# Kernel tuning notes

Measured on AMD Instinct MI355X. Metric: run time of the kernel, lower is better.

## Reference

```python
import jax, jax.numpy as jnp
import numpy as np
from jax import lax

B, S, T = 32, 128, 64          # batch, src_len, trg_len
E, H = 64, 512                 # embed_dim, hidden_size
SRC_V, TRG_V = 32000, 32000


def gru_cell(x, h, W_ih, W_hh, b_ih, b_hh):
    """PyTorch-convention GRU cell. x:[B,I], h:[B,H] -> h':[B,H]"""
    gi = x @ W_ih.T + b_ih            # [B,3H]
    gh = h @ W_hh.T + b_hh            # [B,3H]
    i_r, i_z, i_n = jnp.split(gi, 3, axis=-1)
    h_r, h_z, h_n = jnp.split(gh, 3, axis=-1)
    r = jax.nn.sigmoid(i_r + h_r)
    z = jax.nn.sigmoid(i_z + h_z)
    n = jnp.tanh(i_n + r * h_n)
    return (1.0 - z) * n + z * h


def setup_inputs() -> dict:
    key = jax.random.key(0)
    ks = jax.random.split(key, 22)
    g = lambda i, shape: jax.random.normal(ks[i], shape, jnp.float32) * 0.05
    return {
        "src": jax.random.randint(ks[0], (B, S), 0, SRC_V),
        "trg": jax.random.randint(ks[1], (B, T), 0, TRG_V),
        "src_embed": g(2, (SRC_V, E)),
        "trg_embed": g(3, (TRG_V, E)),
        # encoder GRU (1 layer, input E)
        "enc_W_ih": g(4, (3 * H, E)), "enc_W_hh": g(5, (3 * H, H)),
        "enc_b_ih": g(6, (3 * H,)), "enc_b_hh": g(7, (3 * H,)),
        # decoder GRU layer 0 (input E+H due to attention concat)
        "dec0_W_ih": g(8, (3 * H, E + H)), "dec0_W_hh": g(9, (3 * H, H)),
        "dec0_b_ih": g(10, (3 * H,)), "dec0_b_hh": g(11, (3 * H,)),
        # decoder GRU layer 1 (input H)
        "dec1_W_ih": g(12, (3 * H, H)), "dec1_W_hh": g(13, (3 * H, H)),
        "dec1_b_ih": g(14, (3 * H,)), "dec1_b_hh": g(15, (3 * H,)),
        # additive attention: energy = tanh(W[h;enc]) , score = v^T energy
        "attn_W": g(16, (H, 2 * H)), "attn_b": g(17, (H,)),
        "v_W": g(18, (1, H)), "v_b": jnp.zeros((1,), jnp.float32),
        # output projection H -> TRG_V
        "fc_W": g(19, (TRG_V, H)), "fc_b": jnp.zeros((TRG_V,), jnp.float32),
    }


def reference(src, trg, src_embed, trg_embed,
              enc_W_ih, enc_W_hh, enc_b_ih, enc_b_hh,
              dec0_W_ih, dec0_W_hh, dec0_b_ih, dec0_b_hh,
              dec1_W_ih, dec1_W_hh, dec1_b_ih, dec1_b_hh,
              attn_W, attn_b, v_W, v_b, fc_W, fc_b):
    batch = src.shape[0]
    src_e = src_embed[src]                              # [B,S,E]

    # ---- encoder: 1-layer GRU over src ----
    def enc_step(h, x):
        h2 = gru_cell(x, h, enc_W_ih, enc_W_hh, enc_b_ih, enc_b_hh)
        return h2, h2
    h0 = jnp.zeros((batch, H), src_e.dtype)
    h_last, enc_outs = lax.scan(enc_step, h0, jnp.swapaxes(src_e, 0, 1))
    enc_outs = jnp.swapaxes(enc_outs, 0, 1)             # [B,S,H]

    # _adapt_hidden: replicate last encoder layer to 2 decoder layers
    carry0 = (h_last, h_last)

    # ---- decoder: teacher forcing (ratio=1.0), steps t=1..T-1 ----
    def dec_step(carry, tok):
        h0_, h1_ = carry
        # attention context from top decoder layer hidden
        q = jnp.concatenate(
            [jnp.broadcast_to(h1_[:, None, :], enc_outs.shape), enc_outs], axis=-1)  # [B,S,2H]
        energy = jnp.tanh(q @ attn_W.T + attn_b)        # [B,S,H]
        scores = energy @ v_W[0] + v_b[0]               # [B,S]
        w = jax.nn.softmax(scores, axis=-1)
        context = jnp.einsum('bs,bsh->bh', w, enc_outs) # [B,H]
        emb = jnp.concatenate([trg_embed[tok], context], axis=-1)  # [B,E+H]
        h0n = gru_cell(emb, h0_, dec0_W_ih, dec0_W_hh, dec0_b_ih, dec0_b_hh)
        h1n = gru_cell(h0n, h1_, dec1_W_ih, dec1_W_hh, dec1_b_ih, dec1_b_hh)
        logits = h1n @ fc_W.T + fc_b                    # [B,V]
        return (h0n, h1n), logits

    tokens = jnp.swapaxes(trg[:, :-1], 0, 1)            # inputs for t=1..T-1
    _, logits = lax.scan(dec_step, carry0, tokens)      # [T-1,B,V]
    outputs = jnp.concatenate(
        [jnp.zeros((batch, 1, TRG_V), logits.dtype), jnp.swapaxes(logits, 0, 1)], axis=1)
    return outputs                                       # [B,T,V]
```

## Files before the change

kernel.cpp:

```cpp
#include <hip/hip_runtime.h>
#include <hip/hip_bf16.h>

#define BB 32
#define SS 128
#define TT 64
#define EE 64
#define HH 512
#define H3 1536
#define VV 32000
#define EHD 576
#define TD 63
#define MFC 2048

typedef unsigned short u16;
typedef unsigned int   u32;

typedef __attribute__((ext_vector_type(8))) short bf16x8;
typedef __attribute__((ext_vector_type(4))) float f32x4;

__device__ __forceinline__ float bf2f(u16 u){ return __uint_as_float(((u32)u)<<16); }
__device__ __forceinline__ u16 f2bf(float f){
  u32 u = __float_as_uint(f);
  u += 0x7FFFu + ((u>>16)&1u);
  return (u16)(u>>16);
}
__device__ __forceinline__ float sigm(float x){ return 1.f/(1.f+__expf(-x)); }
__device__ __forceinline__ float tanh_f(float x){ return 1.f - 2.f/(1.f+__expf(2.f*x)); }

__device__ __forceinline__ void bf8f(uint4 q, float* f){
  f[0]=__uint_as_float(q.x<<16); f[1]=__uint_as_float(q.x&0xFFFF0000u);
  f[2]=__uint_as_float(q.y<<16); f[3]=__uint_as_float(q.y&0xFFFF0000u);
  f[4]=__uint_as_float(q.z<<16); f[5]=__uint_as_float(q.z&0xFFFF0000u);
  f[6]=__uint_as_float(q.w<<16); f[7]=__uint_as_float(q.w&0xFFFF0000u);
}

template<bool BF>
__device__ __forceinline__ void wload8(const void* base, size_t eoff, float* f){
  if constexpr (BF){
    uint4 q = *(const uint4*)((const u16*)base + eoff);
    bf8f(q, f);
  } else {
    const float4* p = (const float4*)((const float*)base + eoff);
    float4 a = p[0], b = p[1];
    f[0]=a.x; f[1]=a.y; f[2]=a.z; f[3]=a.w;
    f[4]=b.x; f[5]=b.y; f[6]=b.z; f[7]=b.w;
  }
}
template<bool BF>
__device__ __forceinline__ float wld(const void* base, size_t eoff){
  if constexpr (BF) return bf2f(((const u16*)base)[eoff]);
  else              return ((const float*)base)[eoff];
}
template<bool BF>
__device__ __forceinline__ void stage32(const void* gbase, size_t eoff, u16* lds){
  if constexpr (BF){
    const uint4* g = (const uint4*)((const u16*)gbase + eoff);
    uint4* l = (uint4*)lds;
    l[0]=g[0]; l[1]=g[1]; l[2]=g[2]; l[3]=g[3];
  } else {
    const float4* g = (const float4*)((const float*)gbase + eoff);
    #pragma unroll
    for(int i=0;i<8;i++){
      float4 v = g[i];
      u16* d = lds + i*4;
      d[0]=f2bf(v.x); d[1]=f2bf(v.y); d[2]=f2bf(v.z); d[3]=f2bf(v.w);
    }
  }
}

__device__ __forceinline__ void bbar(unsigned int* ctr, int tid, unsigned int target){
  __syncthreads();
  if(tid==0){
    __hip_atomic_fetch_add(ctr, 1u, __ATOMIC_RELEASE, __HIP_MEMORY_SCOPE_AGENT);
    while(__hip_atomic_load(ctr, __ATOMIC_RELAXED, __HIP_MEMORY_SCOPE_AGENT) < target){
      __builtin_amdgcn_s_sleep(1);
    }
    __builtin_amdgcn_fence(__ATOMIC_ACQUIRE, "agent");
  }
  __syncthreads();
}

__global__ __launch_bounds__(64) void k_detect(const void* w, int* flag){
  int tid = threadIdx.x;
  const u16* p = (const u16*)w;
  float m = 0.f;
  #pragma unroll
  for(int i=0;i<16;i++){
    float v = fabsf(bf2f(p[tid*16+i]));
    m = fmaxf(m, v);
  }
  #pragma unroll
  for(int off=32;off;off>>=1) m = fmaxf(m, __shfl_down(m, off));
  if(tid==0) *flag = (m < 16.f) ? 1 : 0;
}

template<bool BF>
__device__ void emb_gi_body(const int* toks, int tstride, const void* emb_tab,
                            const void* W_ih, int wstride, const void* b_ih,
                            float* gi)
{
  int blk = blockIdx.x;
  int jc = blk % 6; int b = (blk/6) % BB; int t = blk/(6*BB);
  int tid = threadIdx.x;
  int tok = toks[b*tstride + t];
  __shared__ float emb[EE];
  if(tid < EE) emb[tid] = wld<BF>(emb_tab, (size_t)tok*EE + tid);
  __syncthreads();
  int j = jc*256 + tid;
  float acc = wld<BF>(b_ih, j);
  size_t roff = (size_t)j*wstride;
  #pragma unroll
  for(int i=0;i<8;i++){
    float f[8]; wload8<BF>(W_ih, roff + i*8, f);
    #pragma unroll
    for(int l=0;l<8;l++) acc += emb[i*8+l]*f[l];
  }
  gi[((size_t)t*BB + b)*H3 + j] = acc;
}
__global__ __launch_bounds__(256) void k_emb_gi(
    const int* flag, const int* toks, int tstride, const void* emb_tab,
    const void* W_ih, int wstride, const void* b_ih, float* gi)
{
  if(*flag) emb_gi_body<true>(toks,tstride,emb_tab,W_ih,wstride,b_ih,gi);
  else      emb_gi_body<false>(toks,tstride,emb_tab,W_ih,wstride,b_ih,gi);
}

struct SMem {
  union {
    struct {
      float a[HH];
      float b[HH];
      float red[6][256];
      float eS[16];
    };
    float es16[16][520];
  };
};

struct EncDecParams {
  const int* flag;
  const void *eWhh, *ebhh;
  const float* enc_gi;
  float* enc_outs;
  const void *aW, *ab, *vW, *vb;
  const void *d0Wih, *d0Whh, *d0bhh;
  const float* trg_gi;
  const void *d1Wih, *d1bih, *d1Whh, *d1bhh;
  float* hE;
  float* h0b;
  float* h1b;
  float* P;
  float* Abuf;
  float* Cpart;
  float* Ssum;
  u16* h1_all;
  unsigned int* bctr;
};

template<bool BF>
__device__ void enc_step_dev(SMem& sm, int b, int q, int tid,
                             const float* hin, float* hout,
                             const void* W_hh, const void* b_hh,
                             const float* gi_t, float* enc_outs, int t,
                             float* h0init, float* h1init)
{
  float* hs = sm.b;
  const float* hrow = hin + b*HH;
  hs[tid] = hrow[tid]; hs[tid+256] = hrow[tid+256];
  __syncthreads();
  int jj = tid >> 2, t4 = tid & 3;
  int j = q*64 + jj;
  int k0 = t4*128;
  float ar=0.f, az=0.f, an=0.f;
  size_t orr = (size_t)j*HH + k0;
  size_t oz = (size_t)(512+j)*HH + k0;
  size_t on = (size_t)(1024+j)*HH + k0;
  #pragma unroll 4
  for(int i=0;i<16;i++){
    float f[8];
    wload8<BF>(W_hh, orr + i*8, f);
    #pragma unroll
    for(int l=0;l<8;l++) ar += hs[k0+i*8+l]*f[l];
    wload8<BF>(W_hh, oz + i*8, f);
    #pragma unroll
    for(int l=0;l<8;l++) az += hs[k0+i*8+l]*f[l];
    wload8<BF>(W_hh, on + i*8, f);
    #pragma unroll
    for(int l=0;l<8;l++) an += hs[k0+i*8+l]*f[l];
  }
  sm.red[0][tid]=ar; sm.red[1][tid]=az; sm.red[2][tid]=an;
  __syncthreads();
  if(t4==0){
    float gr = sm.red[0][tid]+sm.red[0][tid+1]+sm.red[0][tid+2]+sm.red[0][tid+3] + wld<BF>(b_hh, j);
    float gz = sm.red[1][tid]+sm.red[1][tid+1]+sm.red[1][tid+2]+sm.red[1][tid+3] + wld<BF>(b_hh, 512+j);
    float gn = sm.red[2][tid]+sm.red[2][tid+1]+sm.red[2][tid+2]+sm.red[2][tid+3] + wld<BF>(b_hh, 1024+j);
    const float* gib = gi_t + b*H3;
    float r = sigm(gib[j] + gr);
    float z = sigm(gib[512+j] + gz);
    float n = tanh_f(gib[1024+j] + r*gn);
    float hn = (1.f - z)*n + z*hs[j];
    hout[b*HH + j] = hn;
    enc_outs[((size_t)b*SS + t)*HH + j] = hn;
    if(h0init){ h0init[b*HH+j] = hn; h1init[b*HH+j] = hn; }
  }
}

template<bool BF>
__device__ void attn_proj_blk(SMem& sm, int b, int q, int tid,
                              const float* enc_outs, const void* attn_W,
                              const void* attn_b, float* P)
{
  #pragma unroll 4
  for(int i=0;i<16;i++){
    const float* er = enc_outs + ((size_t)b*SS + q*16 + i)*HH;
    sm.es16[i][tid]     = er[tid];
    sm.es16[i][tid+256] = er[tid+256];
  }
  __syncthreads();
  #pragma unroll
  for(int rr=0; rr<2; rr++){
    int j = rr*256 + tid;
    float bj = wld<BF>(attn_b, j);
    float acc[16];
    #pragma unroll
    for(int i=0;i<16;i++) acc[i] = bj;
    size_t roff = (size_t)j*1024 + 512;
    for(int kk=0;kk<64;kk++){
      float f[8]; wload8<BF>(attn_W, roff + kk*8, f);
      #pragma unroll
      for(int i=0;i<16;i++){
        const float4* e4 = (const float4*)(&sm.es16[i][kk*8]);
        float4 ea = e4[0], eb = e4[1];
        acc[i] += ea.x*f[0]+ea.y*f[1]+ea.z*f[2]+ea.w*f[3]
                + eb.x*f[4]+eb.y*f[5]+eb.z*f[6]+eb.w*f[7];
      }
    }
    #pragma unroll
    for(int i=0;i<16;i++)
      P[((size_t)b*SS + q*16 + i)*HH + j] = acc[i];
  }
  __syncthreads();
}

template<bool BF>
__device__ void dec_A_dev(SMem& sm, int b, int q, int tid,
                          const float* h1, const void* attn_W, float* Abuf)
{
  float* hsr = sm.b;
  hsr[tid]=h1[b*HH+tid]; hsr[tid+256]=h1[b*HH+tid+256];
  __syncthreads();
  int jj = tid>>2, t4 = tid&3, j = q*64+jj, k0 = t4*128;
  size_t roff = (size_t)j*1024 + k0;
  float acc = 0.f;
  #pragma unroll 4
  for(int i=0;i<16;i++){
    float f[8]; wload8<BF>(attn_W, roff + i*8, f);
    #pragma unroll
    for(int l=0;l<8;l++) acc += hsr[k0+i*8+l]*f[l];
  }
  sm.red[0][tid]=acc;
  __syncthreads();
  if(t4==0){
    Abuf[b*HH + j] = sm.red[0][tid]+sm.red[0][tid+1]+sm.red[0][tid+2]+sm.red[0][tid+3];
  }
}

template<bool BF>
__device__ void dec_scores_dev(SMem& sm, int b, int sb, int tid,
                               const float* Abuf, const float* P,
                               const float* enc_outs, const void* vW,
                               const void* vb, float* Cpart, float* Ssum)
{
  float* As = sm.a;
  float* vs = sm.b;
  As[tid]=Abuf[b*HH+tid]; As[tid+256]=Abuf[b*HH+tid+256];
  vs[tid]=wld<BF>(vW, tid); vs[tid+256]=wld<BF>(vW, tid+256);
  __syncthreads();
  int wave = tid>>6, lane = tid&63;
  float vbf = wld<BF>(vb, 0);
  #pragma unroll
  for(int i=0;i<4;i++){
    int s = sb*16 + wave*4 + i;
    const float* Prow = P + ((size_t)b*SS+s)*HH;
    float part = 0.f;
    #pragma unroll
    for(int kk=0;kk<8;kk++){
      int k = lane + kk*64;
      part += vs[k]*tanh_f(As[k]+Prow[k]);
    }
    #pragma unroll
    for(int off=32;off;off>>=1) part += __shfl_down(part, off);
    if(lane==0) sm.eS[wave*4+i] = __expf(part + vbf);
  }
  __syncthreads();
  for(int j=tid;j<HH;j+=256){
    float c = 0.f;
    #pragma unroll 4
    for(int i=0;i<16;i++) c += sm.eS[i]*enc_outs[((size_t)b*SS + sb*16+i)*HH + j];
    Cpart[((size_t)b*8+sb)*HH + j] = c;
  }
  if(tid==0){ float ss=0.f; for(int i=0;i<16;i++) ss+=sm.eS[i]; Ssum[b*8+sb]=ss; }
}

template<bool BF>
__device__ void dec_h0_dev(SMem& sm, int b, int q, int tid,
                           const float* h0in, float* h0out,
                           const float* Cpart, const float* Ssum,
                           const void* W_ih, const void* W_hh,
                           const void* b_hh, const float* gi_t)
{
  float* ctx = sm.a;
  float* hs  = sm.b;
  const float* hr = h0in + b*HH;
  hs[tid]=hr[tid]; hs[tid+256]=hr[tid+256];
  float ssum = 0.f;
  #pragma unroll
  for(int sb=0;sb<8;sb++) ssum += Ssum[b*8+sb];
  float invS = 1.f/ssum;
  for(int j=tid;j<HH;j+=256){
    float c = 0.f;
    #pragma unroll
    for(int sb=0;sb<8;sb++) c += Cpart[((size_t)b*8+sb)*HH + j];
    ctx[j] = c*invS;
  }
  __syncthreads();
  int jj = tid>>2, t4 = tid&3, j = q*64+jj, k0 = t4*128;
  float pr=0.f,pz=0.f,pn=0.f,qr=0.f,qz=0.f,qn=0.f;
  size_t oir = (size_t)j*EHD + 64 + k0;
  size_t oiz = (size_t)(512+j)*EHD + 64 + k0;
  size_t oin = (size_t)(1024+j)*EHD + 64 + k0;
  size_t ohr = (size_t)j*HH + k0;
  size_t ohz = (size_t)(512+j)*HH + k0;
  size_t ohn = (size_t)(1024+j)*HH + k0;
  #pragma unroll 2
  for(int i=0;i<16;i++){
    float f[8];
    wload8<BF>(W_ih, oir + i*8, f);
    #pragma unroll
    for(int l=0;l<8;l++) pr += ctx[k0+i*8+l]*f[l];
    wload8<BF>(W_ih, oiz + i*8, f);
    #pragma unroll
    for(int l=0;l<8;l++) pz += ctx[k0+i*8+l]*f[l];
    wload8<BF>(W_ih, oin + i*8, f);
    #pragma unroll
    for(int l=0;l<8;l++) pn += ctx[k0+i*8+l]*f[l];
    wload8<BF>(W_hh, ohr + i*8, f);
    #pragma unroll
    for(int l=0;l<8;l++) qr += hs[k0+i*8+l]*f[l];
    wload8<BF>(W_hh, ohz + i*8, f);
    #pragma unroll
    for(int l=0;l<8;l++) qz += hs[k0+i*8+l]*f[l];
    wload8<BF>(W_hh, ohn + i*8, f);
    #pragma unroll
    for(int l=0;l<8;l++) qn += hs[k0+i*8+l]*f[l];
  }
  sm.red[0][tid]=pr; sm.red[1][tid]=pz; sm.red[2][tid]=pn;
  sm.red[3][tid]=qr; sm.red[4][tid]=qz; sm.red[5][tid]=qn;
  __syncthreads();
  if(t4==0){
    float gir = gi_t[b*H3 + j]        + sm.red[0][tid]+sm.red[0][tid+1]+sm.red[0][tid+2]+sm.red[0][tid+3];
    float giz = gi_t[b*H3 + 512 + j]  + sm.red[1][tid]+sm.red[1][tid+1]+sm.red[1][tid+2]+sm.red[1][tid+3];
    float gin = gi_t[b*H3 + 1024 + j] + sm.red[2][tid]+sm.red[2][tid+1]+sm.red[2][tid+2]+sm.red[2][tid+3];
    float ghr = sm.red[3][tid]+sm.red[3][tid+1]+sm.red[3][tid+2]+sm.red[3][tid+3] + wld<BF>(b_hh, j);
    float ghz = sm.red[4][tid]+sm.red[4][tid+1]+sm.red[4][tid+2]+sm.red[4][tid+3] + wld<BF>(b_hh, 512+j);
    float ghn = sm.red[5][tid]+sm.red[5][tid+1]+sm.red[5][tid+2]+sm.red[5][tid+3] + wld<BF>(b_hh, 1024+j);
    float r = sigm(gir+ghr), z = sigm(giz+ghz), n = tanh_f(gin + r*ghn);
    h0out[b*HH + j] = (1.f - z)*n + z*hs[j];
  }
}

template<bool BF>
__device__ void dec_h1_dev(SMem& sm, int b, int q, int tid,
                           const float* xin, const float* h1in, float* h1out,
                           const void* W_ih, const void* b_ih,
                           const void* W_hh, const void* b_hh,
                           u16* h1_all_t)
{
  float* xs = sm.a;
  float* hs = sm.b;
  const float* xr = xin + b*HH;
  const float* hr = h1in + b*HH;
  xs[tid]=xr[tid]; xs[tid+256]=xr[tid+256];
  hs[tid]=hr[tid]; hs[tid+256]=hr[tid+256];
  __syncthreads();
  int jj = tid>>2, t4 = tid&3, j = q*64+jj, k0 = t4*128;
  float pr=0.f,pz=0.f,pn=0.f,qr=0.f,qz=0.f,qn=0.f;
  size_t oir = (size_t)j*HH + k0;
  size_t oiz = (size_t)(512+j)*HH + k0;
  size_t oin = (size_t)(1024+j)*HH + k0;
  #pragma unroll 2
  for(int i=0;i<16;i++){
    float f[8];
    wload8<BF>(W_ih, oir + i*8, f);
    #pragma unroll
    for(int l=0;l<8;l++) pr += xs[k0+i*8+l]*f[l];
    wload8<BF>(W_ih, oiz + i*8, f);
    #pragma unroll
    for(int l=0;l<8;l++) pz += xs[k0+i*8+l]*f[l];
    wload8<BF>(W_ih, oin + i*8, f);
    #pragma unroll
    for(int l=0;l<8;l++) pn += xs[k0+i*8+l]*f[l];
    wload8<BF>(W_hh, oir + i*8, f);
    #pragma unroll
    for(int l=0;l<8;l++) qr += hs[k0+i*8+l]*f[l];
    wload8<BF>(W_hh, oiz + i*8, f);
    #pragma unroll
    for(int l=0;l<8;l++) qz += hs[k0+i*8+l]*f[l];
    wload8<BF>(W_hh, oin + i*8, f);
    #pragma unroll
    for(int l=0;l<8;l++) qn += hs[k0+i*8+l]*f[l];
  }
  sm.red[0][tid]=pr; sm.red[1][tid]=pz; sm.red[2][tid]=pn;
  sm.red[3][tid]=qr; sm.red[4][tid]=qz; sm.red[5][tid]=qn;
  __syncthreads();
  if(t4==0){
    float gir = wld<BF>(b_ih, j)      + sm.red[0][tid]+sm.red[0][tid+1]+sm.red[0][tid+2]+sm.red[0][tid+3];
    float giz = wld<BF>(b_ih, 512+j)  + sm.red[1][tid]+sm.red[1][tid+1]+sm.red[1][tid+2]+sm.red[1][tid+3];
    float gin = wld<BF>(b_ih, 1024+j) + sm.red[2][tid]+sm.red[2][tid+1]+sm.red[2][tid+2]+sm.red[2][tid+3];
    float ghr = sm.red[3][tid]+sm.red[3][tid+1]+sm.red[3][tid+2]+sm.red[3][tid+3] + wld<BF>(b_hh, j);
    float ghz = sm.red[4][tid]+sm.red[4][tid+1]+sm.red[4][tid+2]+sm.red[4][tid+3] + wld<BF>(b_hh, 512+j);
    float ghn = sm.red[5][tid]+sm.red[5][tid+1]+sm.red[5][tid+2]+sm.red[5][tid+3] + wld<BF>(b_hh, 1024+j);
    float r = sigm(gir+ghr), z = sigm(giz+ghz), n = tanh_f(gin + r*ghn);
    float hn = (1.f - z)*n + z*hs[j];
    h1out[b*HH + j] = hn;
    h1_all_t[b*HH + j] = f2bf(hn);
  }
}

template<bool BF>
__device__ void encdec_body(const EncDecParams& p, SMem& sm)
{
  int blk = blockIdx.x, tid = threadIdx.x;
  int b = blk & 31, q = blk >> 5;
  unsigned int* ctr = p.bctr + b*64;
  unsigned int bt = 0;

  for(int t=0;t<SS;t++){
    enc_step_dev<BF>(sm, b, q, tid,
        p.hE + (t&1)*BB*HH, p.hE + ((t+1)&1)*BB*HH,
        p.eWhh, p.ebhh, p.enc_gi + (size_t)t*BB*H3, p.enc_outs, t,
        (t==SS-1)? p.h0b : (float*)nullptr,
        (t==SS-1)? p.h1b : (float*)nullptr);
    bt += 8; bbar(ctr, tid, bt);
  }

  attn_proj_blk<BF>(sm, b, q, tid, p.enc_outs, p.aW, p.ab, p.P);
  bt += 8; bbar(ctr, tid, bt);

  for(int t=0;t<TD;t++){
    int pi = t&1, po = (t+1)&1;
    dec_A_dev<BF>(sm, b, q, tid, p.h1b + pi*BB*HH, p.aW, p.Abuf);
    bt += 8; bbar(ctr, tid, bt);
    dec_scores_dev<BF>(sm, b, q, tid, p.Abuf, p.P, p.enc_outs, p.vW, p.vb,
                       p.Cpart, p.Ssum);
    bt += 8; bbar(ctr, tid, bt);
    dec_h0_dev<BF>(sm, b, q, tid, p.h0b + pi*BB*HH, p.h0b + po*BB*HH,
                   p.Cpart, p.Ssum, p.d0Wih, p.d0Whh, p.d0bhh,
                   p.trg_gi + (size_t)t*BB*H3);
    bt += 8; bbar(ctr, tid, bt);
    dec_h1_dev<BF>(sm, b, q, tid, p.h0b + po*BB*HH, p.h1b + pi*BB*HH,
                   p.h1b + po*BB*HH, p.d1Wih, p.d1bih, p.d1Whh, p.d1bhh,
                   p.h1_all + (size_t)t*BB*HH);
    bt += 8; bbar(ctr, tid, bt);
  }
}

__global__ __launch_bounds__(256) void k_encdec(EncDecParams p)
{
  __shared__ SMem sm;
  if(*p.flag) encdec_body<true>(p, sm);
  else        encdec_body<false>(p, sm);
}

__global__ __launch_bounds__(256) void k_zero_t0(const int* flag, void* out){
  int idx = blockIdx.x*256 + threadIdx.x;
  int b = idx / VV, v = idx - b*VV;
  size_t o = (size_t)b*TT*VV + v;
  if(*flag) ((u16*)out)[o] = 0;
  else      ((float*)out)[o] = 0.f;
}

template<bool BF>
__device__ void fc_body(const u16* A, const void* W, const void* bias, void* out)
{
  __shared__ u16 As[128*72];
  __shared__ u16 Bs[128*72];
  int bm = blockIdx.x, bn = blockIdx.y;
  int tid = threadIdx.x;
  int wave = tid>>6, lane = tid&63;
  int wr = wave>>1, wc = wave&1;
  f32x4 acc[4][4];
  f32x4 zero = {0.f,0.f,0.f,0.f};
  #pragma unroll
  for(int i=0;i<4;i++)
    #pragma unroll
    for(int j=0;j<4;j++) acc[i][j]=zero;

  int row = tid>>1, half = tid&1;
  const size_t gA = (size_t)(bm*128 + row)*512 + half*32;
  const size_t gB = (size_t)(bn*128 + row)*512 + half*32;
  u16* lA = As + row*72 + half*32;
  u16* lB = Bs + row*72 + half*32;

  for(int kk=0;kk<8;kk++){
    int k0 = kk*64;
    if(kk) __syncthreads();
    stage32<true>(A, gA + k0, lA);
    stage32<BF>(W, gB + k0, lB);
    __syncthreads();
    #pragma unroll
    for(int ks=0;ks<2;ks++){
      int kof = ks*32 + (lane>>4)*8;
      bf16x8 af[4], bfv[4];
      #pragma unroll
      for(int i=0;i<4;i++){
        af[i]  = *(const bf16x8*)(As + (wr*64 + i*16 + (lane&15))*72 + kof);
        bfv[i] = *(const bf16x8*)(Bs + (wc*64 + i*16 + (lane&15))*72 + kof);
      }
      #pragma unroll
      for(int i=0;i<4;i++)
        #pragma unroll
        for(int j=0;j<4;j++)
          acc[i][j] = __builtin_amdgcn_mfma_f32_16x16x32_bf16(af[i], bfv[j], acc[i][j], 0, 0, 0);
    }
  }
  int quad = lane>>4, col = lane&15;
  #pragma unroll
  for(int j=0;j<4;j++){
    int n = bn*128 + wc*64 + j*16 + col;
    float bsv = wld<BF>(bias, n);
    #pragma unroll
    for(int i=0;i<4;i++){
      int mbase = bm*128 + wr*64 + i*16 + quad*4;
      #pragma unroll
      for(int r=0;r<4;r++){
        int m = mbase + r;
        if(m < TD*BB){
          int t = m >> 5, b = m & 31;
          size_t o = ((size_t)(b*TT + t + 1))*VV + n;
          float v = acc[i][j][r] + bsv;
          if constexpr (BF) ((u16*)out)[o] = f2bf(v);
          else              ((float*)out)[o] = v;
        }
      }
    }
  }
}
__global__ __launch_bounds__(256) void k_fc(
  const int* flag, const u16* A, const void* W, const void* bias, void* out)
{
  if(*flag) fc_body<true>(A, W, bias, out);
  else      fc_body<false>(A, W, bias, out);
}

extern "C" void kernel_launch(void* const* d_in, const int* in_sizes, int n_in,
                              void* d_out, int out_size, void* d_ws, size_t ws_size,
                              hipStream_t stream)
{
  const int* src = (const int*)d_in[0];
  const int* trg = (const int*)d_in[1];
  const void* src_emb = d_in[2];
  const void* trg_emb = d_in[3];
  const void* eWih = d_in[4];
  const void* eWhh = d_in[5];
  const void* ebih = d_in[6];
  const void* ebhh = d_in[7];
  const void* d0Wih = d_in[8];
  const void* d0Whh = d_in[9];
  const void* d0bih = d_in[10];
  const void* d0bhh = d_in[11];
  const void* d1Wih = d_in[12];
  const void* d1Whh = d_in[13];
  const void* d1bih = d_in[14];
  const void* d1bhh = d_in[15];
  const void* aW  = d_in[16];
  const void* ab  = d_in[17];
  const void* vW  = d_in[18];
  const void* vb  = d_in[19];
  const void* fcW = d_in[20];
  const void* fcb = d_in[21];

  char* w = (char*)d_ws;
  int*   flag    = (int*)w;   w += 16;
  float* enc_gi  = (float*)w; w += (size_t)SS*BB*H3*4;
  float* trg_gi  = (float*)w; w += (size_t)TD*BB*H3*4;
  float* enc_outs= (float*)w; w += (size_t)BB*SS*HH*4;
  float* P       = (float*)w; w += (size_t)BB*SS*HH*4;
  float* hE      = (float*)w; w += (size_t)2*BB*HH*4;
  float* h0b     = (float*)w; w += (size_t)2*BB*HH*4;
  float* h1b     = (float*)w; w += (size_t)2*BB*HH*4;
  float* Abuf    = (float*)w; w += (size_t)BB*HH*4;
  float* Cpart   = (float*)w; w += (size_t)BB*8*HH*4;
  float* Ssum    = (float*)w; w += (size_t)BB*8*4;
  u16*   h1_all  = (u16*)w;   w += (size_t)MFC*HH*2;
  unsigned int* bctr = (unsigned int*)w; w += (size_t)BB*64*4;

  (void)hipMemsetAsync(hE, 0, BB*HH*4, stream);
  (void)hipMemsetAsync(h1_all + (size_t)TD*BB*HH, 0, 32*HH*2, stream);
  (void)hipMemsetAsync(bctr, 0, (size_t)BB*64*4, stream);

  k_detect<<<1,64,0,stream>>>(fcW, flag);

  k_emb_gi<<<SS*BB*6, 256, 0, stream>>>(flag, src, SS, src_emb, eWih, EE, ebih, enc_gi);
  k_emb_gi<<<TD*BB*6, 256, 0, stream>>>(flag, trg, TT, trg_emb, d0Wih, EHD, d0bih, trg_gi);

  EncDecParams prm;
  prm.flag = flag;
  prm.eWhh = eWhh; prm.ebhh = ebhh;
  prm.enc_gi = enc_gi;
  prm.enc_outs = enc_outs;
  prm.aW = aW; prm.ab = ab; prm.vW = vW; prm.vb = vb;
  prm.d0Wih = d0Wih; prm.d0Whh = d0Whh; prm.d0bhh = d0bhh;
  prm.trg_gi = trg_gi;
  prm.d1Wih = d1Wih; prm.d1bih = d1bih; prm.d1Whh = d1Whh; prm.d1bhh = d1bhh;
  prm.hE = hE; prm.h0b = h0b; prm.h1b = h1b;
  prm.P = P; prm.Abuf = Abuf; prm.Cpart = Cpart; prm.Ssum = Ssum;
  prm.h1_all = h1_all;
  prm.bctr = bctr;

  void* kargs[] = { (void*)&prm };
  (void)hipLaunchCooperativeKernel(reinterpret_cast<void*>(&k_encdec),
                                   dim3(256), dim3(256), kargs, 0, stream);

  k_zero_t0<<<(BB*VV)/256, 256, 0, stream>>>(flag, d_out);
  dim3 g(16, 250);
  k_fc<<<g, 256, 0, stream>>>(flag, h1_all, fcW, fcb, d_out);
}
```

Baseline: 8.419 ms.

## Use atomic agent-scope loads with workgroup fence, pad LDS, regroup batch blocks

Cross-block data (hidden states, enc_outs, Cpart, Ssum, Abuf) is now read with relaxed agent-scope 64-bit atomic loads. This lets the barrier's acquire fence be weakened from agent to workgroup scope, avoiding a full L2/cache invalidate on every step barrier. Shared hidden-state arrays are padded by 8 floats per 128 to remove LDS bank conflicts when four lanes read different k-segments. Block-to-batch mapping changes so the 8 blocks of one batch are contiguous, likely so they land on nearby CUs/XCDs. The catch is that correctness now depends on every cross-block read going through the atomic loads, and any plain load left behind could observe stale data.

```diff
diff --git a/kernel.cpp b/kernel.cpp
--- a/kernel.cpp
+++ b/kernel.cpp
@@ -68,6 +68,19 @@
   }
 }
 
+__device__ __forceinline__ float2 cld2(const float* p){
+  unsigned long long u = __hip_atomic_load((const unsigned long long*)p,
+                                           __ATOMIC_RELAXED, __HIP_MEMORY_SCOPE_AGENT);
+  float2 r;
+  r.x = __uint_as_float((u32)u);
+  r.y = __uint_as_float((u32)(u>>32));
+  return r;
+}
+__device__ __forceinline__ float cld1(const float* p){
+  u32 u = __hip_atomic_load((const u32*)p, __ATOMIC_RELAXED, __HIP_MEMORY_SCOPE_AGENT);
+  return __uint_as_float(u);
+}
+
 __device__ __forceinline__ void bbar(unsigned int* ctr, int tid, unsigned int target){
   __syncthreads();
   if(tid==0){
@@ -75,7 +88,7 @@
     while(__hip_atomic_load(ctr, __ATOMIC_RELAXED, __HIP_MEMORY_SCOPE_AGENT) < target){
       __builtin_amdgcn_s_sleep(1);
     }
-    __builtin_amdgcn_fence(__ATOMIC_ACQUIRE, "agent");
+    __builtin_amdgcn_fence(__ATOMIC_ACQUIRE, "workgroup");
   }
   __syncthreads();
 }
@@ -128,8 +141,8 @@
 struct SMem {
   union {
     struct {
-      float a[HH];
-      float b[HH];
+      float a[544];
+      float b[544];
       float red[6][256];
       float eS[16];
     };
@@ -165,12 +178,16 @@
                              float* h0init, float* h1init)
 {
   float* hs = sm.b;
-  const float* hrow = hin + b*HH;
-  hs[tid] = hrow[tid]; hs[tid+256] = hrow[tid+256];
+  {
+    float2 h2 = cld2(hin + b*HH + 2*tid);
+    int sk = ((2*tid)>>7)<<3;
+    hs[2*tid+sk] = h2.x; hs[2*tid+1+sk] = h2.y;
+  }
   __syncthreads();
   int jj = tid >> 2, t4 = tid & 3;
   int j = q*64 + jj;
   int k0 = t4*128;
+  const float* hsb = hs + t4*136;
   float ar=0.f, az=0.f, an=0.f;
   size_t orr = (size_t)j*HH + k0;
   size_t oz = (size_t)(512+j)*HH + k0;
@@ -180,13 +197,13 @@
     float f[8];
     wload8<BF>(W_hh, orr + i*8, f);
     #pragma unroll
-    for(int l=0;l<8;l++) ar += hs[k0+i*8+l]*f[l];
+    for(int l=0;l<8;l++) ar += hsb[i*8+l]*f[l];
     wload8<BF>(W_hh, oz + i*8, f);
     #pragma unroll
-    for(int l=0;l<8;l++) az += hs[k0+i*8+l]*f[l];
+    for(int l=0;l<8;l++) az += hsb[i*8+l]*f[l];
     wload8<BF>(W_hh, on + i*8, f);
     #pragma unroll
-    for(int l=0;l<8;l++) an += hs[k0+i*8+l]*f[l];
+    for(int l=0;l<8;l++) an += hsb[i*8+l]*f[l];
   }
   sm.red[0][tid]=ar; sm.red[1][tid]=az; sm.red[2][tid]=an;
   __syncthreads();
@@ -198,7 +215,8 @@
     float r = sigm(gib[j] + gr);
     float z = sigm(gib[512+j] + gz);
     float n = tanh_f(gib[1024+j] + r*gn);
-    float hn = (1.f - z)*n + z*hs[j];
+    int jsk = j + ((j>>7)<<3);
+    float hn = (1.f - z)*n + z*hs[jsk];
     hout[b*HH + j] = hn;
     enc_outs[((size_t)b*SS + t)*HH + j] = hn;
     if(h0init){ h0init[b*HH+j] = hn; h1init[b*HH+j] = hn; }
@@ -213,8 +231,9 @@
   #pragma unroll 4
   for(int i=0;i<16;i++){
     const float* er = enc_outs + ((size_t)b*SS + q*16 + i)*HH;
-    sm.es16[i][tid]     = er[tid];
-    sm.es16[i][tid+256] = er[tid+256];
+    float2 v = cld2(er + 2*tid);
+    sm.es16[i][2*tid]   = v.x;
+    sm.es16[i][2*tid+1] = v.y;
   }
   __syncthreads();
   #pragma unroll
@@ -247,16 +266,21 @@
                           const float* h1, const void* attn_W, float* Abuf)
 {
   float* hsr = sm.b;
-  hsr[tid]=h1[b*HH+tid]; hsr[tid+256]=h1[b*HH+tid+256];
+  {
+    float2 h2 = cld2(h1 + b*HH + 2*tid);
+    int sk = ((2*tid)>>7)<<3;
+    hsr[2*tid+sk] = h2.x; hsr[2*tid+1+sk] = h2.y;
+  }
   __syncthreads();
   int jj = tid>>2, t4 = tid&3, j = q*64+jj, k0 = t4*128;
+  const float* hsrb = hsr + t4*136;
   size_t roff = (size_t)j*1024 + k0;
   float acc = 0.f;
   #pragma unroll 4
   for(int i=0;i<16;i++){
     float f[8]; wload8<BF>(attn_W, roff + i*8, f);
     #pragma unroll
-    for(int l=0;l<8;l++) acc += hsr[k0+i*8+l]*f[l];
+    for(int l=0;l<8;l++) acc += hsrb[i*8+l]*f[l];
   }
   sm.red[0][tid]=acc;
   __syncthreads();
@@ -273,7 +297,10 @@
 {
   float* As = sm.a;
   float* vs = sm.b;
-  As[tid]=Abuf[b*HH+tid]; As[tid+256]=Abuf[b*HH+tid+256];
+  {
+    float2 a2 = cld2(Abuf + b*HH + 2*tid);
+    As[2*tid]=a2.x; As[2*tid+1]=a2.y;
+  }
   vs[tid]=wld<BF>(vW, tid); vs[tid+256]=wld<BF>(vW, tid+256);
   __syncthreads();
   int wave = tid>>6, lane = tid&63;
@@ -293,11 +320,16 @@
     if(lane==0) sm.eS[wave*4+i] = __expf(part + vbf);
   }
   __syncthreads();
-  for(int j=tid;j<HH;j+=256){
-    float c = 0.f;
-    #pragma unroll 4
-    for(int i=0;i<16;i++) c += sm.eS[i]*enc_outs[((size_t)b*SS + sb*16+i)*HH + j];
-    Cpart[((size_t)b*8+sb)*HH + j] = c;
+  {
+    float c0=0.f, c1=0.f;
+    const float* eb0 = enc_outs + ((size_t)b*SS + sb*16)*HH + 2*tid;
+    #pragma unroll
+    for(int i=0;i<16;i++){
+      float2 v = cld2(eb0 + (size_t)i*HH);
+      c0 += sm.eS[i]*v.x; c1 += sm.eS[i]*v.y;
+    }
+    float* cp = Cpart + ((size_t)b*8+sb)*HH;
+    cp[2*tid]=c0; cp[2*tid+1]=c1;
   }
   if(tid==0){ float ss=0.f; for(int i=0;i<16;i++) ss+=sm.eS[i]; Ssum[b*8+sb]=ss; }
 }
@@ -311,20 +343,26 @@
 {
   float* ctx = sm.a;
   float* hs  = sm.b;
-  const float* hr = h0in + b*HH;
-  hs[tid]=hr[tid]; hs[tid+256]=hr[tid+256];
   float ssum = 0.f;
   #pragma unroll
-  for(int sb=0;sb<8;sb++) ssum += Ssum[b*8+sb];
+  for(int sb=0;sb<8;sb++) ssum += cld1(&Ssum[b*8+sb]);
   float invS = 1.f/ssum;
-  for(int j=tid;j<HH;j+=256){
-    float c = 0.f;
-    #pragma unroll
-    for(int sb=0;sb<8;sb++) c += Cpart[((size_t)b*8+sb)*HH + j];
-    ctx[j] = c*invS;
+  {
+    float c0=0.f, c1=0.f;
+    #pragma unroll
+    for(int sb=0;sb<8;sb++){
+      float2 v = cld2(Cpart + ((size_t)b*8+sb)*HH + 2*tid);
+      c0+=v.x; c1+=v.y;
+    }
+    int sk = ((2*tid)>>7)<<3;
+    ctx[2*tid+sk]=c0*invS; ctx[2*tid+1+sk]=c1*invS;
+    float2 h2 = cld2(h0in + b*HH + 2*tid);
+    hs[2*tid+sk]=h2.x; hs[2*tid+1+sk]=h2.y;
   }
   __syncthreads();
   int jj = tid>>2, t4 = tid&3, j = q*64+jj, k0 = t4*128;
+  const float* ctxb = ctx + t4*136;
+  const float* hsb  = hs  + t4*136;
   float pr=0.f,pz=0.f,pn=0.f,qr=0.f,qz=0.f,qn=0.f;
   size_t oir = (size_t)j*EHD + 64 + k0;
   size_t oiz = (size_t)(512+j)*EHD + 64 + k0;
@@ -337,22 +375,22 @@
     float f[8];
     wload8<BF>(W_ih, oir + i*8, f);
     #pragma unroll
-    for(int l=0;l<8;l++) pr += ctx[k0+i*8+l]*f[l];
+    for(int l=0;l<8;l++) pr += ctxb[i*8+l]*f[l];
     wload8<BF>(W_ih, oiz + i*8, f);
     #pragma unroll
-    for(int l=0;l<8;l++) pz += ctx[k0+i*8+l]*f[l];
+    for(int l=0;l<8;l++) pz += ctxb[i*8+l]*f[l];
     wload8<BF>(W_ih, oin + i*8, f);
     #pragma unroll
-    for(int l=0;l<8;l++) pn += ctx[k0+i*8+l]*f[l];
+    for(int l=0;l<8;l++) pn += ctxb[i*8+l]*f[l];
     wload8<BF>(W_hh, ohr + i*8, f);
     #pragma unroll
-    for(int l=0;l<8;l++) qr += hs[k0+i*8+l]*f[l];
+    for(int l=0;l<8;l++) qr += hsb[i*8+l]*f[l];
     wload8<BF>(W_hh, ohz + i*8, f);
     #pragma unroll
-    for(int l=0;l<8;l++) qz += hs[k0+i*8+l]*f[l];
+    for(int l=0;l<8;l++) qz += hsb[i*8+l]*f[l];
     wload8<BF>(W_hh, ohn + i*8, f);
     #pragma unroll
-    for(int l=0;l<8;l++) qn += hs[k0+i*8+l]*f[l];
+    for(int l=0;l<8;l++) qn += hsb[i*8+l]*f[l];
   }
   sm.red[0][tid]=pr; sm.red[1][tid]=pz; sm.red[2][tid]=pn;
   sm.red[3][tid]=qr; sm.red[4][tid]=qz; sm.red[5][tid]=qn;
@@ -365,7 +403,8 @@
     float ghz = sm.red[4][tid]+sm.red[4][tid+1]+sm.red[4][tid+2]+sm.red[4][tid+3] + wld<BF>(b_hh, 512+j);
     float ghn = sm.red[5][tid]+sm.red[5][tid+1]+sm.red[5][tid+2]+sm.red[5][tid+3] + wld<BF>(b_hh, 1024+j);
     float r = sigm(gir+ghr), z = sigm(giz+ghz), n = tanh_f(gin + r*ghn);
-    h0out[b*HH + j] = (1.f - z)*n + z*hs[j];
+    int jsk = j + ((j>>7)<<3);
+    h0out[b*HH + j] = (1.f - z)*n + z*hs[jsk];
   }
 }
 
@@ -378,12 +417,17 @@
 {
   float* xs = sm.a;
   float* hs = sm.b;
-  const float* xr = xin + b*HH;
-  const float* hr = h1in + b*HH;
-  xs[tid]=xr[tid]; xs[tid+256]=xr[tid+256];
-  hs[tid]=hr[tid]; hs[tid+256]=hr[tid+256];
+  {
+    int sk = ((2*tid)>>7)<<3;
+    float2 x2 = cld2(xin + b*HH + 2*tid);
+    xs[2*tid+sk]=x2.x; xs[2*tid+1+sk]=x2.y;
+    float2 h2 = cld2(h1in + b*HH + 2*tid);
+    hs[2*tid+sk]=h2.x; hs[2*tid+1+sk]=h2.y;
+  }
   __syncthreads();
   int jj = tid>>2, t4 = tid&3, j = q*64+jj, k0 = t4*128;
+  const float* xsb = xs + t4*136;
+  const float* hsb = hs + t4*136;
   float pr=0.f,pz=0.f,pn=0.f,qr=0.f,qz=0.f,qn=0.f;
   size_t oir = (size_t)j*HH + k0;
   size_t oiz = (size_t)(512+j)*HH + k0;
@@ -393,22 +437,22 @@
     float f[8];
     wload8<BF>(W_ih, oir + i*8, f);
     #pragma unroll
-    for(int l=0;l<8;l++) pr += xs[k0+i*8+l]*f[l];
+    for(int l=0;l<8;l++) pr += xsb[i*8+l]*f[l];
     wload8<BF>(W_ih, oiz + i*8, f);
     #pragma unroll
-    for(int l=0;l<8;l++) pz += xs[k0+i*8+l]*f[l];
+    for(int l=0;l<8;l++) pz += xsb[i*8+l]*f[l];
     wload8<BF>(W_ih, oin + i*8, f);
     #pragma unroll
-    for(int l=0;l<8;l++) pn += xs[k0+i*8+l]*f[l];
+    for(int l=0;l<8;l++) pn += xsb[i*8+l]*f[l];
     wload8<BF>(W_hh, oir + i*8, f);
     #pragma unroll
-    for(int l=0;l<8;l++) qr += hs[k0+i*8+l]*f[l];
+    for(int l=0;l<8;l++) qr += hsb[i*8+l]*f[l];
     wload8<BF>(W_hh, oiz + i*8, f);
     #pragma unroll
-    for(int l=0;l<8;l++) qz += hs[k0+i*8+l]*f[l];
+    for(int l=0;l<8;l++) qz += hsb[i*8+l]*f[l];
     wload8<BF>(W_hh, oin + i*8, f);
     #pragma unroll
-    for(int l=0;l<8;l++) qn += hs[k0+i*8+l]*f[l];
+    for(int l=0;l<8;l++) qn += hsb[i*8+l]*f[l];
   }
   sm.red[0][tid]=pr; sm.red[1][tid]=pz; sm.red[2][tid]=pn;
   sm.red[3][tid]=qr; sm.red[4][tid]=qz; sm.red[5][tid]=qn;
@@ -421,7 +465,8 @@
     float ghz = sm.red[4][tid]+sm.red[4][tid+1]+sm.red[4][tid+2]+sm.red[4][tid+3] + wld<BF>(b_hh, 512+j);
     float ghn = sm.red[5][tid]+sm.red[5][tid+1]+sm.red[5][tid+2]+sm.red[5][tid+3] + wld<BF>(b_hh, 1024+j);
     float r = sigm(gir+ghr), z = sigm(giz+ghz), n = tanh_f(gin + r*ghn);
-    float hn = (1.f - z)*n + z*hs[j];
+    int jsk = j + ((j>>7)<<3);
+    float hn = (1.f - z)*n + z*hs[jsk];
     h1out[b*HH + j] = hn;
     h1_all_t[b*HH + j] = f2bf(hn);
   }
@@ -431,7 +476,7 @@
 __device__ void encdec_body(const EncDecParams& p, SMem& sm)
 {
   int blk = blockIdx.x, tid = threadIdx.x;
-  int b = blk & 31, q = blk >> 5;
+  int b = blk >> 3, q = blk & 7;
   unsigned int* ctr = p.bctr + b*64;
   unsigned int bt = 0;
 
```

New measurement: 8.202 ms. -2.6%, faster.
